# Kernel tuning notes

Hardware: AMD Instinct MI355X
Metric: run time of the kernel (lower is better)

## Reference

```python
import jax, jax.numpy as jnp
import numpy as np
from jax import lax

BN_EPS = 1e-5

def _conv1d_same(x, w):
    # x: [N, 1, C], w: [1, 1, k] with k odd -> SAME padding along channel axis
    k = w.shape[-1]
    return lax.conv_general_dilated(x, w, window_strides=(1,),
                                    padding=[(k // 2, k // 2)],
                                    dimension_numbers=('NCH', 'OIH', 'NCH'))

def setup_inputs() -> dict:
    key = jax.random.key(0)
    ks = jax.random.split(key, 6)
    B, C, H, W = 4, 64, 64, 64
    kk = 3  # kernel size from in_dim=64: t=int(abs(log2(64)+1)/2)=3 (odd)
    x = jax.random.normal(ks[0], (B, C, H, W), dtype=jnp.float32)
    q_w = jax.random.normal(ks[1], (1, 1, kk), dtype=jnp.float32) * 0.5
    k_w = jax.random.normal(ks[2], (1, 1, kk), dtype=jnp.float32) * 0.5
    v_w = jax.random.normal(ks[3], (C, C), dtype=jnp.float32) * (1.0 / np.sqrt(C))
    v_b = jnp.zeros((C,), dtype=jnp.float32)
    gamma = jax.random.uniform(ks[4], (1,), dtype=jnp.float32, minval=0.5, maxval=1.5)
    bn_w = jnp.ones((C,), dtype=jnp.float32)
    bn_b = jnp.zeros((C,), dtype=jnp.float32)
    return {"x": x, "q_w": q_w, "k_w": k_w, "v_w": v_w, "v_b": v_b,
            "gamma": gamma, "bn_w": bn_w, "bn_b": bn_b}

def reference(x, q_w, k_w, v_w, v_b, gamma, bn_w, bn_b):
    B, C, H, W = x.shape
    N = H * W
    # conv1d Q/K projections over the channel axis, per spatial position
    xp = x.reshape(B, C, N).transpose(0, 2, 1).reshape(B * N, 1, C)
    q = _conv1d_same(xp, q_w).reshape(B, N, C)   # proj_query: [B, HW, C]
    k = _conv1d_same(xp, k_w).reshape(B, N, C)   # proj_key (pre-permute)
    energy = jnp.einsum('bnc,bmc->bnm', q, k)    # [B, HW, HW]
    attn = jax.nn.softmax(energy, axis=-1)
    # 1x1 value conv
    v = jnp.einsum('oc,bchw->bohw', v_w, x) + v_b[None, :, None, None]
    vv = v.reshape(B, C, N)
    # bmm(value, attention^T)
    out = jnp.einsum('bcm,bnm->bcn', vv, attn).reshape(B, C, H, W)
    y = gamma[0] * out
    # BatchNorm2d, training mode (batch statistics, biased variance)
    mean = jnp.mean(y, axis=(0, 2, 3), keepdims=True)
    var = jnp.var(y, axis=(0, 2, 3), keepdims=True)
    y = (y - mean) * lax.rsqrt(var + BN_EPS)
    y = y * bn_w[None, :, None, None] + bn_b[None, :, None, None]
    return y + x
```

## Files before the change

kernel.cpp:

```cpp
#include <hip/hip_runtime.h>
#include <stdint.h>

using f16 = _Float16;

typedef _Float16 f16x8 __attribute__((ext_vector_type(8)));
typedef _Float16 f16x4 __attribute__((ext_vector_type(4)));
typedef float f32x4 __attribute__((ext_vector_type(4)));

#define LOG2E 1.44269504088896340736f

__device__ __forceinline__ f16 f2h(float f) { return (f16)f; }

#if __has_builtin(__builtin_amdgcn_exp2f)
__device__ __forceinline__ float fexp2(float x) { return __builtin_amdgcn_exp2f(x); }
#else
__device__ __forceinline__ float fexp2(float x) { return exp2f(x); }
#endif

typedef __attribute__((address_space(1))) const uint32_t gu32;
typedef __attribute__((address_space(3))) uint32_t lu32;

__device__ __forceinline__ void dma16(const void* g, void* l) {
  __builtin_amdgcn_global_load_lds((gu32*)g, (lu32*)l, 16, 0, 0);
}

__device__ __forceinline__ f16x8 cvt8(const float* p) {
  const float4 a = *(const float4*)p;
  const float4 b = *(const float4*)(p + 4);
  f16x8 r;
  r[0] = (f16)a.x; r[1] = (f16)a.y; r[2] = (f16)a.z; r[3] = (f16)a.w;
  r[4] = (f16)b.x; r[5] = (f16)b.y; r[6] = (f16)b.z; r[7] = (f16)b.w;
  return r;
}


__global__ __launch_bounds__(256, 2) void pam_pre(
    const float* __restrict__ x, const float* __restrict__ qw,
    const float* __restrict__ kw, const float* __restrict__ vw,
    const float* __restrict__ vb,
    f16* __restrict__ qa, f16* __restrict__ ka2, f16* __restrict__ va3,
    float* __restrict__ gz)
{
  __shared__ alignas(16) f16 xt[16 * 72];
  const int tid = threadIdx.x;
  const int b = blockIdx.x >> 8;
  const int n0 = (blockIdx.x & 255) << 4;
  const int lane = tid & 63;
  const int wv = tid >> 6;
  const int quad = lane >> 4, l15 = lane & 15;

  if (blockIdx.x == 0 && tid < 128) gz[tid] = 0.f;

  {
    const int c = tid >> 2;
    const int j0 = (tid & 3) << 2;
    const float4 v0 = *(const float4*)(x + ((size_t)(b * 64 + c) << 12) + n0 + j0);
    xt[(j0 + 0) * 72 + c] = f2h(v0.x);
    xt[(j0 + 1) * 72 + c] = f2h(v0.y);
    xt[(j0 + 2) * 72 + c] = f2h(v0.z);
    xt[(j0 + 3) * 72 + c] = f2h(v0.w);
  }
  __syncthreads();

  if (tid < 128) {
    const float qw0 = qw[0], qw1 = qw[1], qw2 = qw[2];
    const float kw0 = kw[0], kw1 = kw[1], kw2 = kw[2];
    const int n = tid >> 3;
    const int c8 = tid & 7;
    const f16x8 v0 = *(const f16x8*)&xt[n * 72 + c8 * 8];
    const float lm = (c8 > 0) ? (float)xt[n * 72 + c8 * 8 - 1] : 0.f;
    const float rp = (c8 < 7) ? (float)xt[n * 72 + c8 * 8 + 8] : 0.f;
    f16x8 qv8, kv8;
#pragma unroll
    for (int j = 0; j < 8; ++j) {
      const float xm = (j == 0) ? lm : (float)v0[j - 1];
      const float x0 = (float)v0[j];
      const float xp = (j == 7) ? rp : (float)v0[j + 1];
      qv8[j] = f2h((qw0 * xm + qw1 * x0 + qw2 * xp) * LOG2E);
      kv8[j] = f2h(kw0 * xm + kw1 * x0 + kw2 * xp);
    }
    const int nn = n0 + n;
    *(f16x8*)(qa + ((size_t)((b << 12) + nn) << 6) + c8 * 8) = qv8;
    const int np = nn ^ ((((nn >> 3) & 1) << 2) | ((nn >> 4) & 1));
    *(f16x8*)(ka2 + (((size_t)(b * 8 + c8)) << 15) + (np << 3)) = kv8;
  }

  {
    const f16x8 a0 = *(const f16x8*)&xt[l15 * 72 + quad * 8];
    const f16x8 a1 = *(const f16x8*)&xt[l15 * 72 + quad * 8 + 32];
    const int co = wv * 16 + l15;
    const f16x8 b0 = cvt8(vw + co * 64 + quad * 8);
    const f16x8 b1 = cvt8(vw + co * 64 + quad * 8 + 32);
    f32x4 z = {0.f, 0.f, 0.f, 0.f};
    z = __builtin_amdgcn_mfma_f32_16x16x32_f16(a0, b0, z, 0, 0, 0);
    z = __builtin_amdgcn_mfma_f32_16x16x32_f16(a1, b1, z, 0, 0, 0);
    const float vbv = vb[co];
    f16x4 pv;
#pragma unroll
    for (int r = 0; r < 4; ++r) pv[r] = f2h(z[r] + vbv);
    const int nb = n0 + quad * 4;
    *(f16x4*)(va3 + (((size_t)(b * 512 + (nb >> 3))) << 9)
              + (co << 3) + (nb & 7)) = pv;
  }
}

__global__ __launch_bounds__(512, 4) void pam_attn(
    const f16* __restrict__ qa, const f16* __restrict__ ka2,
    const f16* __restrict__ va3, const float* __restrict__ gam,
    float* __restrict__ y0, float* __restrict__ gs1, float* __restrict__ gs2)
{
  __shared__ alignas(16) f16 kbuf[4][8192];
  __shared__ float ldsO[32 * 65];
  __shared__ float ldsM[4][32], ldsL[4][32], ldsMg[32], ldsInv[32];

  const int tid = threadIdx.x;
  const int wv = tid >> 6, lane = tid & 63;
  const int quad = lane >> 4, l15 = lane & 15;
  const int ks = wv & 3, qh = wv >> 2;
  const int b = blockIdx.x & 3;
  const int qb = blockIdx.x >> 2;
  const int qb0 = qb << 5;
  const int phase = qb & 31;

  for (int i = tid; i < 32 * 65; i += 512) ldsO[i] = 0.f;

  const int bn = b << 12;
  f16x8 bq0, bq1;
  {
    const int q = qb0 + qh * 16 + l15;
    const f16* qp = qa + ((size_t)(bn + q) << 6) + quad * 8;
    bq0 = *(const f16x8*)qp;
    bq1 = *(const f16x8*)(qp + 32);
  }

  const f16* kg0 = ka2 + (((size_t)(b * 8 + wv)) << 15) + (lane << 3);
  const f16* vgp = va3 + ((size_t)b << 18) + ((ks * 4 + quad) << 9) + (l15 << 3);

  f32x4 o[4] = {};
  float m = -1e30f, lp = 0.f;

  {
    const int g0 = phase;
    const int g1 = (1 + phase) & 31;
    dma16(kg0 + ((size_t)g0 << 10),       kbuf[0] + (wv << 10));
    dma16(kg0 + ((size_t)g0 << 10) + 512, kbuf[0] + (wv << 10) + 512);
    dma16(kg0 + ((size_t)g1 << 10),       kbuf[1] + (wv << 10));
    dma16(kg0 + ((size_t)g1 << 10) + 512, kbuf[1] + (wv << 10) + 512);
  }
  asm volatile("s_waitcnt vmcnt(2)" ::: "memory");
  __builtin_amdgcn_s_barrier();

  const int u = l15 >> 2;
  const int xmsk = ((u & 1) << 2) | (u >> 1);
  const int pos0 = (ks << 5) + (u << 3) + (l15 & 3);
  const int koff0 = (pos0 ^ xmsk) << 3;
  const int koff1 = koff0 ^ 32;

#pragma unroll 1
  for (int kt = 0; kt < 32; ++kt) {
    const int cur = kt & 3;
    const int gcur = (kt + phase) & 31;

    const f16* vt = vgp + ((size_t)gcur << 13);
    const f16x8 av0 = *(const f16x8*)(vt);
    const f16x8 av1 = *(const f16x8*)(vt + 128);
    const f16x8 av2 = *(const f16x8*)(vt + 256);
    const f16x8 av3 = *(const f16x8*)(vt + 384);
    __builtin_amdgcn_sched_barrier(0);

    if (kt < 30) {
      const int tn = (kt + 2 + phase) & 31;
      f16* kd = kbuf[(kt + 2) & 3] + (wv << 10);
      dma16(kg0 + ((size_t)tn << 10),       kd);
      dma16(kg0 + ((size_t)tn << 10) + 512, kd + 512);
    }

    const f16* kc = kbuf[cur];
    const f16x8 ak00 = *(const f16x8*)(kc + (quad << 10) + koff0);
    const f16x8 ak01 = *(const f16x8*)(kc + ((4 + quad) << 10) + koff0);
    const f16x8 ak10 = *(const f16x8*)(kc + (quad << 10) + koff1);
    const f16x8 ak11 = *(const f16x8*)(kc + ((4 + quad) << 10) + koff1);

    f32x4 z0, z1;
    {
      f32x4 z = {0.f, 0.f, 0.f, 0.f};
      z = __builtin_amdgcn_mfma_f32_16x16x32_f16(ak00, bq0, z, 0, 0, 0);
      z0 = __builtin_amdgcn_mfma_f32_16x16x32_f16(ak01, bq1, z, 0, 0, 0);
    }
    {
      f32x4 z = {0.f, 0.f, 0.f, 0.f};
      z = __builtin_amdgcn_mfma_f32_16x16x32_f16(ak10, bq0, z, 0, 0, 0);
      z1 = __builtin_amdgcn_mfma_f32_16x16x32_f16(ak11, bq1, z, 0, 0, 0);
    }

    float tmax = fmaxf(fmaxf(fmaxf(z0[0], z0[1]), fmaxf(z0[2], z0[3])),
                       fmaxf(fmaxf(z1[0], z1[1]), fmaxf(z1[2], z1[3])));
    tmax = fmaxf(tmax, __shfl_xor(tmax, 16, 64));
    tmax = fmaxf(tmax, __shfl_xor(tmax, 32, 64));
    const bool need = !__all(tmax <= m + 8.f);
    const float mn = need ? fmaxf(m, tmax) : m;

    const float p0 = fexp2(z0[0] - mn);
    const float p1 = fexp2(z0[1] - mn);
    const float p2 = fexp2(z0[2] - mn);
    const float p3 = fexp2(z0[3] - mn);
    const float p4 = fexp2(z1[0] - mn);
    const float p5 = fexp2(z1[1] - mn);
    const float p6 = fexp2(z1[2] - mn);
    const float p7 = fexp2(z1[3] - mn);
    const float ts = ((p0 + p1) + (p2 + p3)) + ((p4 + p5) + (p6 + p7));

    f16x8 pa;
    pa[0] = f2h(p0); pa[1] = f2h(p1); pa[2] = f2h(p2); pa[3] = f2h(p3);
    pa[4] = f2h(p4); pa[5] = f2h(p5); pa[6] = f2h(p6); pa[7] = f2h(p7);

    if (need) {
      const float al = fexp2(m - mn);
      lp = lp * al + ts;
      m = mn;
#pragma unroll
      for (int ct = 0; ct < 4; ++ct)
        for (int r = 0; r < 4; ++r) o[ct][r] *= al;
    } else {
      lp += ts;
    }

    o[0] = __builtin_amdgcn_mfma_f32_16x16x32_f16(av0, pa, o[0], 0, 0, 0);
    o[1] = __builtin_amdgcn_mfma_f32_16x16x32_f16(av1, pa, o[1], 0, 0, 0);
    o[2] = __builtin_amdgcn_mfma_f32_16x16x32_f16(av2, pa, o[2], 0, 0, 0);
    o[3] = __builtin_amdgcn_mfma_f32_16x16x32_f16(av3, pa, o[3], 0, 0, 0);

    asm volatile("s_waitcnt vmcnt(2)" ::: "memory");
    __builtin_amdgcn_s_barrier();
  }

  asm volatile("s_waitcnt vmcnt(0)" ::: "memory");

  {
    float v = lp;
    v += __shfl_xor(v, 16, 64);
    v += __shfl_xor(v, 32, 64);
    if (quad == 0) {
      ldsM[ks][qh * 16 + l15] = m;
      ldsL[ks][qh * 16 + l15] = v;
    }
  }
  __syncthreads();

  if (tid < 32) {
    const float M = fmaxf(fmaxf(ldsM[0][tid], ldsM[1][tid]),
                          fmaxf(ldsM[2][tid], ldsM[3][tid]));
    const float lt = ldsL[0][tid] * fexp2(ldsM[0][tid] - M) +
                     ldsL[1][tid] * fexp2(ldsM[1][tid] - M) +
                     ldsL[2][tid] * fexp2(ldsM[2][tid] - M) +
                     ldsL[3][tid] * fexp2(ldsM[3][tid] - M);
    ldsMg[tid] = M;
    ldsInv[tid] = 1.f / lt;
  }
  __syncthreads();

  {
    const int q = qh * 16 + l15;
    const float sc = fexp2(m - ldsMg[q]);
#pragma unroll
    for (int ct = 0; ct < 4; ++ct)
      for (int r = 0; r < 4; ++r)
        atomicAdd(&ldsO[q * 65 + ct * 16 + quad * 4 + r], o[ct][r] * sc);
  }
  __syncthreads();

  const float g = gam[0];
  {
    const int c = tid >> 3;
    const int q0 = (tid & 7) << 2;
    float4 v4;
    float* vp = &v4.x;
    float s1 = 0.f, s2 = 0.f;
    for (int r = 0; r < 4; ++r) {
      const float val = g * ldsO[(q0 + r) * 65 + c] * ldsInv[q0 + r];
      vp[r] = val; s1 += val; s2 += val * val;
    }
    *(float4*)(y0 + ((size_t)(b * 64 + c) << 12) + qb0 + q0) = v4;
    s1 += __shfl_xor(s1, 1, 64);
    s2 += __shfl_xor(s2, 1, 64);
    s1 += __shfl_xor(s1, 2, 64);
    s2 += __shfl_xor(s2, 2, 64);
    s1 += __shfl_xor(s1, 4, 64);
    s2 += __shfl_xor(s2, 4, 64);
    if ((tid & 7) == 0) {
      atomicAdd(&gs1[c], s1);
      atomicAdd(&gs2[c], s2);
    }
  }
}

__global__ __launch_bounds__(256, 2) void pam_apply(
    const float* __restrict__ y0, const float* __restrict__ x,
    const float* __restrict__ gs1, const float* __restrict__ gs2,
    const float* __restrict__ bnw, const float* __restrict__ bnb,
    float* __restrict__ out)
{
  const int i = (blockIdx.x * 256 + threadIdx.x) << 2;
  const int c = (i >> 12) & 63;
  const float inv_n = 1.f / 16384.f;
  const float mean = gs1[c] * inv_n;
  const float var = fmaxf(gs2[c] * inv_n - mean * mean, 0.f);
  const float sc = bnw[c] * rsqrtf(var + 1e-5f);
  const float sh = bnb[c] - mean * sc;
  const float4 y = *(const float4*)(y0 + i);
  const float4 xv = *(const float4*)(x + i);
  float4 r;
  r.x = y.x * sc + sh + xv.x;
  r.y = y.y * sc + sh + xv.y;
  r.z = y.z * sc + sh + xv.z;
  r.w = y.w * sc + sh + xv.w;
  *(float4*)(out + i) = r;
}

extern "C" void kernel_launch(void* const* d_in, const int* in_sizes, int n_in,
                              void* d_out, int out_size, void* d_ws, size_t ws_size,
                              hipStream_t stream)
{
  (void)in_sizes; (void)n_in; (void)out_size; (void)ws_size;
  const float* x   = (const float*)d_in[0];
  const float* qw  = (const float*)d_in[1];
  const float* kw  = (const float*)d_in[2];
  const float* vw  = (const float*)d_in[3];
  const float* vb  = (const float*)d_in[4];
  const float* gam = (const float*)d_in[5];
  const float* bnw = (const float*)d_in[6];
  const float* bnb = (const float*)d_in[7];

  char* ws = (char*)d_ws;
  f16*   qa  = (f16*)(ws);
  f16*   ka2 = (f16*)(ws + (2u << 20));
  f16*   va3 = (f16*)(ws + (4u << 20));
  float* y0  = (float*)(ws + (6u << 20));
  float* gs1 = (float*)(ws + (10u << 20));
  float* gs2 = (float*)(ws + (10u << 20) + 256);

  pam_pre  <<<1024, 256, 0, stream>>>(x, qw, kw, vw, vb, qa, ka2, va3, gs1);
  pam_attn <<<512, 512, 0, stream>>>(qa, ka2, va3, gam, y0, gs1, gs2);
  pam_apply<<<1024, 256, 0, stream>>>(y0, x, gs1, gs2, bnw, bnb, (float*)d_out);
}
```

Measured before the change: 148.2 us.

## Process two key tiles per iteration with independent softmax states

The attention loop now handles two K/V tiles per iteration, with separate running max, sum and output accumulators (A and B) that are merged at the end through an 8-way LDS reduction. This halves the number of block barriers and gives the scheduler two independent MFMA/exp chains to interleave, meant to hide latency. The DMA prefetch now issues two tiles one iteration ahead, and the explicit vmcnt waits are replaced by __syncthreads. The cost is more accumulator registers, which may hurt occupancy under the launch bounds of 512 threads and 4 blocks.

```diff
diff --git a/kernel.cpp b/kernel.cpp
--- a/kernel.cpp
+++ b/kernel.cpp
@@ -111,7 +111,7 @@
 {
   __shared__ alignas(16) f16 kbuf[4][8192];
   __shared__ float ldsO[32 * 65];
-  __shared__ float ldsM[4][32], ldsL[4][32], ldsMg[32], ldsInv[32];
+  __shared__ float ldsM[8][32], ldsL[8][32], ldsMg[32], ldsInv[32];
 
   const int tid = threadIdx.x;
   const int wv = tid >> 6, lane = tid & 63;
@@ -120,7 +120,6 @@
   const int b = blockIdx.x & 3;
   const int qb = blockIdx.x >> 2;
   const int qb0 = qb << 5;
-  const int phase = qb & 31;
 
   for (int i = tid; i < 32 * 65; i += 512) ldsO[i] = 0.f;
 
@@ -136,19 +135,17 @@
   const f16* kg0 = ka2 + (((size_t)(b * 8 + wv)) << 15) + (lane << 3);
   const f16* vgp = va3 + ((size_t)b << 18) + ((ks * 4 + quad) << 9) + (l15 << 3);
 
-  f32x4 o[4] = {};
-  float m = -1e30f, lp = 0.f;
-
-  {
-    const int g0 = phase;
-    const int g1 = (1 + phase) & 31;
+  f32x4 oA[4] = {}, oB[4] = {};
+  float mA = -1e30f, lpA = 0.f, mB = -1e30f, lpB = 0.f;
+
+  {
+    const int g0 = (qb & 15) << 1, g1 = g0 | 1;
     dma16(kg0 + ((size_t)g0 << 10),       kbuf[0] + (wv << 10));
     dma16(kg0 + ((size_t)g0 << 10) + 512, kbuf[0] + (wv << 10) + 512);
     dma16(kg0 + ((size_t)g1 << 10),       kbuf[1] + (wv << 10));
     dma16(kg0 + ((size_t)g1 << 10) + 512, kbuf[1] + (wv << 10) + 512);
   }
-  asm volatile("s_waitcnt vmcnt(2)" ::: "memory");
-  __builtin_amdgcn_s_barrier();
+  __syncthreads();
 
   const int u = l15 >> 2;
   const int xmsk = ((u & 1) << 2) | (u >> 1);
@@ -157,103 +154,145 @@
   const int koff1 = koff0 ^ 32;
 
 #pragma unroll 1
-  for (int kt = 0; kt < 32; ++kt) {
-    const int cur = kt & 3;
-    const int gcur = (kt + phase) & 31;
-
-    const f16* vt = vgp + ((size_t)gcur << 13);
-    const f16x8 av0 = *(const f16x8*)(vt);
-    const f16x8 av1 = *(const f16x8*)(vt + 128);
-    const f16x8 av2 = *(const f16x8*)(vt + 256);
-    const f16x8 av3 = *(const f16x8*)(vt + 384);
-    __builtin_amdgcn_sched_barrier(0);
-
-    if (kt < 30) {
-      const int tn = (kt + 2 + phase) & 31;
-      f16* kd = kbuf[(kt + 2) & 3] + (wv << 10);
-      dma16(kg0 + ((size_t)tn << 10),       kd);
-      dma16(kg0 + ((size_t)tn << 10) + 512, kd + 512);
-    }
-
-    const f16* kc = kbuf[cur];
-    const f16x8 ak00 = *(const f16x8*)(kc + (quad << 10) + koff0);
-    const f16x8 ak01 = *(const f16x8*)(kc + ((4 + quad) << 10) + koff0);
-    const f16x8 ak10 = *(const f16x8*)(kc + (quad << 10) + koff1);
-    const f16x8 ak11 = *(const f16x8*)(kc + ((4 + quad) << 10) + koff1);
-
-    f32x4 z0, z1;
+  for (int p = 0; p < 16; ++p) {
+    const int sA = (2 * p) & 3, sB = (2 * p + 1) & 3;
+    const int pr = (p + qb) & 15;
+    const int gA = pr << 1, gB = gA | 1;
+
+    if (p < 15) {
+      const int prn = (p + 1 + qb) & 15;
+      const int gnA = prn << 1, gnB = gnA | 1;
+      f16* kdA = kbuf[(2 * p + 2) & 3] + (wv << 10);
+      f16* kdB = kbuf[(2 * p + 3) & 3] + (wv << 10);
+      dma16(kg0 + ((size_t)gnA << 10),       kdA);
+      dma16(kg0 + ((size_t)gnA << 10) + 512, kdA + 512);
+      dma16(kg0 + ((size_t)gnB << 10),       kdB);
+      dma16(kg0 + ((size_t)gnB << 10) + 512, kdB + 512);
+    }
+
+    const f16* vtA = vgp + ((size_t)gA << 13);
+    const f16x8 avA0 = *(const f16x8*)(vtA);
+    const f16x8 avA1 = *(const f16x8*)(vtA + 128);
+    const f16x8 avA2 = *(const f16x8*)(vtA + 256);
+    const f16x8 avA3 = *(const f16x8*)(vtA + 384);
+    const f16* vtB = vgp + ((size_t)gB << 13);
+    const f16x8 avB0 = *(const f16x8*)(vtB);
+    const f16x8 avB1 = *(const f16x8*)(vtB + 128);
+    const f16x8 avB2 = *(const f16x8*)(vtB + 256);
+    const f16x8 avB3 = *(const f16x8*)(vtB + 384);
+
+    f32x4 zA0, zA1;
     {
+      const f16* kc = kbuf[sA];
+      const f16x8 ak00 = *(const f16x8*)(kc + (quad << 10) + koff0);
+      const f16x8 ak01 = *(const f16x8*)(kc + ((4 + quad) << 10) + koff0);
+      const f16x8 ak10 = *(const f16x8*)(kc + (quad << 10) + koff1);
+      const f16x8 ak11 = *(const f16x8*)(kc + ((4 + quad) << 10) + koff1);
       f32x4 z = {0.f, 0.f, 0.f, 0.f};
       z = __builtin_amdgcn_mfma_f32_16x16x32_f16(ak00, bq0, z, 0, 0, 0);
-      z0 = __builtin_amdgcn_mfma_f32_16x16x32_f16(ak01, bq1, z, 0, 0, 0);
-    }
+      zA0 = __builtin_amdgcn_mfma_f32_16x16x32_f16(ak01, bq1, z, 0, 0, 0);
+      f32x4 y = {0.f, 0.f, 0.f, 0.f};
+      y = __builtin_amdgcn_mfma_f32_16x16x32_f16(ak10, bq0, y, 0, 0, 0);
+      zA1 = __builtin_amdgcn_mfma_f32_16x16x32_f16(ak11, bq1, y, 0, 0, 0);
+    }
+    f32x4 zB0, zB1;
     {
+      const f16* kc = kbuf[sB];
+      const f16x8 ak00 = *(const f16x8*)(kc + (quad << 10) + koff0);
+      const f16x8 ak01 = *(const f16x8*)(kc + ((4 + quad) << 10) + koff0);
+      const f16x8 ak10 = *(const f16x8*)(kc + (quad << 10) + koff1);
+      const f16x8 ak11 = *(const f16x8*)(kc + ((4 + quad) << 10) + koff1);
       f32x4 z = {0.f, 0.f, 0.f, 0.f};
-      z = __builtin_amdgcn_mfma_f32_16x16x32_f16(ak10, bq0, z, 0, 0, 0);
-      z1 = __builtin_amdgcn_mfma_f32_16x16x32_f16(ak11, bq1, z, 0, 0, 0);
-    }
-
-    float tmax = fmaxf(fmaxf(fmaxf(z0[0], z0[1]), fmaxf(z0[2], z0[3])),
-                       fmaxf(fmaxf(z1[0], z1[1]), fmaxf(z1[2], z1[3])));
-    tmax = fmaxf(tmax, __shfl_xor(tmax, 16, 64));
-    tmax = fmaxf(tmax, __shfl_xor(tmax, 32, 64));
-    const bool need = !__all(tmax <= m + 8.f);
-    const float mn = need ? fmaxf(m, tmax) : m;
-
-    const float p0 = fexp2(z0[0] - mn);
-    const float p1 = fexp2(z0[1] - mn);
-    const float p2 = fexp2(z0[2] - mn);
-    const float p3 = fexp2(z0[3] - mn);
-    const float p4 = fexp2(z1[0] - mn);
-    const float p5 = fexp2(z1[1] - mn);
-    const float p6 = fexp2(z1[2] - mn);
-    const float p7 = fexp2(z1[3] - mn);
-    const float ts = ((p0 + p1) + (p2 + p3)) + ((p4 + p5) + (p6 + p7));
-
-    f16x8 pa;
-    pa[0] = f2h(p0); pa[1] = f2h(p1); pa[2] = f2h(p2); pa[3] = f2h(p3);
-    pa[4] = f2h(p4); pa[5] = f2h(p5); pa[6] = f2h(p6); pa[7] = f2h(p7);
-
-    if (need) {
-      const float al = fexp2(m - mn);
-      lp = lp * al + ts;
-      m = mn;
-#pragma unroll
-      for (int ct = 0; ct < 4; ++ct)
-        for (int r = 0; r < 4; ++r) o[ct][r] *= al;
-    } else {
-      lp += ts;
-    }
-
-    o[0] = __builtin_amdgcn_mfma_f32_16x16x32_f16(av0, pa, o[0], 0, 0, 0);
-    o[1] = __builtin_amdgcn_mfma_f32_16x16x32_f16(av1, pa, o[1], 0, 0, 0);
-    o[2] = __builtin_amdgcn_mfma_f32_16x16x32_f16(av2, pa, o[2], 0, 0, 0);
-    o[3] = __builtin_amdgcn_mfma_f32_16x16x32_f16(av3, pa, o[3], 0, 0, 0);
-
-    asm volatile("s_waitcnt vmcnt(2)" ::: "memory");
-    __builtin_amdgcn_s_barrier();
-  }
-
-  asm volatile("s_waitcnt vmcnt(0)" ::: "memory");
-
-  {
-    float v = lp;
-    v += __shfl_xor(v, 16, 64);
-    v += __shfl_xor(v, 32, 64);
-    if (quad == 0) {
-      ldsM[ks][qh * 16 + l15] = m;
-      ldsL[ks][qh * 16 + l15] = v;
-    }
+      z = __builtin_amdgcn_mfma_f32_16x16x32_f16(ak00, bq0, z, 0, 0, 0);
+      zB0 = __builtin_amdgcn_mfma_f32_16x16x32_f16(ak01, bq1, z, 0, 0, 0);
+      f32x4 y = {0.f, 0.f, 0.f, 0.f};
+      y = __builtin_amdgcn_mfma_f32_16x16x32_f16(ak10, bq0, y, 0, 0, 0);
+      zB1 = __builtin_amdgcn_mfma_f32_16x16x32_f16(ak11, bq1, y, 0, 0, 0);
+    }
+
+    f16x8 paA;
+    {
+      float tmax = fmaxf(fmaxf(fmaxf(zA0[0], zA0[1]), fmaxf(zA0[2], zA0[3])),
+                         fmaxf(fmaxf(zA1[0], zA1[1]), fmaxf(zA1[2], zA1[3])));
+      tmax = fmaxf(tmax, __shfl_xor(tmax, 16, 64));
+      tmax = fmaxf(tmax, __shfl_xor(tmax, 32, 64));
+      const bool need = !__all(tmax <= mA + 8.f);
+      const float mn = need ? fmaxf(mA, tmax) : mA;
+      const float p0 = fexp2(zA0[0] - mn), p1 = fexp2(zA0[1] - mn);
+      const float p2 = fexp2(zA0[2] - mn), p3 = fexp2(zA0[3] - mn);
+      const float p4 = fexp2(zA1[0] - mn), p5 = fexp2(zA1[1] - mn);
+      const float p6 = fexp2(zA1[2] - mn), p7 = fexp2(zA1[3] - mn);
+      const float ts = ((p0 + p1) + (p2 + p3)) + ((p4 + p5) + (p6 + p7));
+      paA[0] = f2h(p0); paA[1] = f2h(p1); paA[2] = f2h(p2); paA[3] = f2h(p3);
+      paA[4] = f2h(p4); paA[5] = f2h(p5); paA[6] = f2h(p6); paA[7] = f2h(p7);
+      if (need) {
+        const float al = fexp2(mA - mn);
+        lpA = lpA * al + ts;
+        mA = mn;
+#pragma unroll
+        for (int ct = 0; ct < 4; ++ct)
+          for (int r = 0; r < 4; ++r) oA[ct][r] *= al;
+      } else {
+        lpA += ts;
+      }
+    }
+    f16x8 paB;
+    {
+      float tmax = fmaxf(fmaxf(fmaxf(zB0[0], zB0[1]), fmaxf(zB0[2], zB0[3])),
+                         fmaxf(fmaxf(zB1[0], zB1[1]), fmaxf(zB1[2], zB1[3])));
+      tmax = fmaxf(tmax, __shfl_xor(tmax, 16, 64));
+      tmax = fmaxf(tmax, __shfl_xor(tmax, 32, 64));
+      const bool need = !__all(tmax <= mB + 8.f);
+      const float mn = need ? fmaxf(mB, tmax) : mB;
+      const float p0 = fexp2(zB0[0] - mn), p1 = fexp2(zB0[1] - mn);
+      const float p2 = fexp2(zB0[2] - mn), p3 = fexp2(zB0[3] - mn);
+      const float p4 = fexp2(zB1[0] - mn), p5 = fexp2(zB1[1] - mn);
+      const float p6 = fexp2(zB1[2] - mn), p7 = fexp2(zB1[3] - mn);
+      const float ts = ((p0 + p1) + (p2 + p3)) + ((p4 + p5) + (p6 + p7));
+      paB[0] = f2h(p0); paB[1] = f2h(p1); paB[2] = f2h(p2); paB[3] = f2h(p3);
+      paB[4] = f2h(p4); paB[5] = f2h(p5); paB[6] = f2h(p6); paB[7] = f2h(p7);
+      if (need) {
+        const float al = fexp2(mB - mn);
+        lpB = lpB * al + ts;
+        mB = mn;
+#pragma unroll
+        for (int ct = 0; ct < 4; ++ct)
+          for (int r = 0; r < 4; ++r) oB[ct][r] *= al;
+      } else {
+        lpB += ts;
+      }
+    }
+
+    oA[0] = __builtin_amdgcn_mfma_f32_16x16x32_f16(avA0, paA, oA[0], 0, 0, 0);
+    oA[1] = __builtin_amdgcn_mfma_f32_16x16x32_f16(avA1, paA, oA[1], 0, 0, 0);
+    oA[2] = __builtin_amdgcn_mfma_f32_16x16x32_f16(avA2, paA, oA[2], 0, 0, 0);
+    oA[3] = __builtin_amdgcn_mfma_f32_16x16x32_f16(avA3, paA, oA[3], 0, 0, 0);
+    oB[0] = __builtin_amdgcn_mfma_f32_16x16x32_f16(avB0, paB, oB[0], 0, 0, 0);
+    oB[1] = __builtin_amdgcn_mfma_f32_16x16x32_f16(avB1, paB, oB[1], 0, 0, 0);
+    oB[2] = __builtin_amdgcn_mfma_f32_16x16x32_f16(avB2, paB, oB[2], 0, 0, 0);
+    oB[3] = __builtin_amdgcn_mfma_f32_16x16x32_f16(avB3, paB, oB[3], 0, 0, 0);
+
+    __syncthreads();
+  }
+
+  lpA += __shfl_xor(lpA, 16, 64);
+  lpA += __shfl_xor(lpA, 32, 64);
+  lpB += __shfl_xor(lpB, 16, 64);
+  lpB += __shfl_xor(lpB, 32, 64);
+  if (quad == 0) {
+    const int q = qh * 16 + l15;
+    ldsM[ks * 2][q] = mA;  ldsL[ks * 2][q] = lpA;
+    ldsM[ks * 2 + 1][q] = mB;  ldsL[ks * 2 + 1][q] = lpB;
   }
   __syncthreads();
 
   if (tid < 32) {
-    const float M = fmaxf(fmaxf(ldsM[0][tid], ldsM[1][tid]),
-                          fmaxf(ldsM[2][tid], ldsM[3][tid]));
-    const float lt = ldsL[0][tid] * fexp2(ldsM[0][tid] - M) +
-                     ldsL[1][tid] * fexp2(ldsM[1][tid] - M) +
-                     ldsL[2][tid] * fexp2(ldsM[2][tid] - M) +
-                     ldsL[3][tid] * fexp2(ldsM[3][tid] - M);
+    float M = ldsM[0][tid];
+#pragma unroll
+    for (int k = 1; k < 8; ++k) M = fmaxf(M, ldsM[k][tid]);
+    float lt = 0.f;
+#pragma unroll
+    for (int k = 0; k < 8; ++k) lt += ldsL[k][tid] * fexp2(ldsM[k][tid] - M);
     ldsMg[tid] = M;
     ldsInv[tid] = 1.f / lt;
   }
@@ -261,11 +300,13 @@
 
   {
     const int q = qh * 16 + l15;
-    const float sc = fexp2(m - ldsMg[q]);
+    const float scA = fexp2(mA - ldsMg[q]);
+    const float scB = fexp2(mB - ldsMg[q]);
 #pragma unroll
     for (int ct = 0; ct < 4; ++ct)
       for (int r = 0; r < 4; ++r)
-        atomicAdd(&ldsO[q * 65 + ct * 16 + quad * 4 + r], o[ct][r] * sc);
+        atomicAdd(&ldsO[q * 65 + ct * 16 + quad * 4 + r],
+                  oA[ct][r] * scA + oB[ct][r] * scB);
   }
   __syncthreads();
 
```

After: 146.7 us, median of 2. No clear change (-1.0%).
